# Optimization experiments

Hardware: AMD Instinct MI355X
Metric: run time of the kernel (lower is better)

Reference implementation:

```python
import jax, jax.numpy as jnp
import numpy as np

N_NODES = 16384
N_EDGES = 131072
EDGE_DIM = 16
IN_CH = 32
OUT_CH = 32
HID_EDGE = 64
MLP_HID = 64  # int(32 * 2.0)
OUT_FINAL = 10
N_GRAPHS = 64
BN_EPS = 1e-5


def setup_inputs() -> dict:
    key = jax.random.key(0)
    ks = jax.random.split(key, 20)
    s = lambda *sh: 1.0 / np.sqrt(sh[0])
    inp = {
        'x': jax.random.normal(ks[0], (N_NODES, IN_CH), jnp.float32),
        'edge_attr': jax.random.normal(ks[1], (N_EDGES, EDGE_DIM), jnp.float32),
        'edge_index': jax.random.randint(ks[2], (2, N_EDGES), 0, N_NODES, jnp.int64),
        'batch': jnp.sort(jax.random.randint(ks[3], (N_NODES,), 0, N_GRAPHS, jnp.int64)),
    }
    # layer 0: edge MLP (EDGE_DIM->HID_EDGE->IN_CH*OUT_CH), root, bias, BN affine
    inp['w1_0'] = jax.random.normal(ks[4], (EDGE_DIM, HID_EDGE), jnp.float32) * s(EDGE_DIM)
    inp['b1_0'] = jnp.zeros((HID_EDGE,), jnp.float32)
    inp['w2_0'] = jax.random.normal(ks[5], (HID_EDGE, IN_CH * OUT_CH), jnp.float32) * s(HID_EDGE)
    inp['b2_0'] = jnp.zeros((IN_CH * OUT_CH,), jnp.float32)
    inp['root_0'] = jax.random.normal(ks[6], (IN_CH, OUT_CH), jnp.float32) * s(IN_CH)
    inp['bias_0'] = jnp.zeros((OUT_CH,), jnp.float32)
    inp['gamma_0'] = jnp.ones((OUT_CH,), jnp.float32)
    inp['beta_0'] = jnp.zeros((OUT_CH,), jnp.float32)
    # layer 1: edge MLP (EDGE_DIM->HID_EDGE->OUT_CH*OUT_CH)
    inp['w1_1'] = jax.random.normal(ks[7], (EDGE_DIM, HID_EDGE), jnp.float32) * s(EDGE_DIM)
    inp['b1_1'] = jnp.zeros((HID_EDGE,), jnp.float32)
    inp['w2_1'] = jax.random.normal(ks[8], (HID_EDGE, OUT_CH * OUT_CH), jnp.float32) * s(HID_EDGE)
    inp['b2_1'] = jnp.zeros((OUT_CH * OUT_CH,), jnp.float32)
    inp['root_1'] = jax.random.normal(ks[9], (OUT_CH, OUT_CH), jnp.float32) * s(OUT_CH)
    inp['bias_1'] = jnp.zeros((OUT_CH,), jnp.float32)
    inp['gamma_1'] = jnp.ones((OUT_CH,), jnp.float32)
    inp['beta_1'] = jnp.zeros((OUT_CH,), jnp.float32)
    # final MLP (dropout is identity in eval / deterministic reference)
    inp['mlp_w1'] = jax.random.normal(ks[10], (OUT_CH, MLP_HID), jnp.float32) * s(OUT_CH)
    inp['mlp_b1'] = jnp.zeros((MLP_HID,), jnp.float32)
    inp['mlp_w2'] = jax.random.normal(ks[11], (MLP_HID, OUT_FINAL), jnp.float32) * s(MLP_HID)
    inp['mlp_b2'] = jnp.zeros((OUT_FINAL,), jnp.float32)
    return inp


def _nnconv(x, src, dst, edge_attr, w1, b1, w2, b2, root, bias, out_ch):
    # per-edge weight matrices from the edge MLP: [E, in, out]
    h = jax.nn.relu(edge_attr @ w1 + b1)
    W = (h @ w2 + b2).reshape(-1, x.shape[1], out_ch)
    msg = jnp.einsum('ei,eio->eo', x[src], W)  # gather + per-edge matmul
    agg = jax.ops.segment_sum(msg, dst, num_segments=N_NODES)
    cnt = jax.ops.segment_sum(jnp.ones((dst.shape[0], 1), x.dtype), dst, num_segments=N_NODES)
    agg = agg / jnp.maximum(cnt, 1.0)  # scatter-mean (zero-degree nodes -> 0)
    return agg + x @ root + bias


def _bn(x, gamma, beta):
    m = jnp.mean(x, axis=0)
    v = jnp.var(x, axis=0)
    return (x - m) * jax.lax.rsqrt(v + BN_EPS) * gamma + beta


def reference(x, edge_attr, edge_index, batch,
              w1_0, b1_0, w2_0, b2_0, root_0, bias_0, gamma_0, beta_0,
              w1_1, b1_1, w2_1, b2_1, root_1, bias_1, gamma_1, beta_1,
              mlp_w1, mlp_b1, mlp_w2, mlp_b2):
    src, dst = edge_index[0], edge_index[1]
    h = _nnconv(x, src, dst, edge_attr, w1_0, b1_0, w2_0, b2_0, root_0, bias_0, OUT_CH)
    h = jax.nn.relu(_bn(h, gamma_0, beta_0))
    h = _nnconv(h, src, dst, edge_attr, w1_1, b1_1, w2_1, b2_1, root_1, bias_1, OUT_CH)
    h = jax.nn.relu(_bn(h, gamma_1, beta_1))
    # global mean pool over graphs
    pooled = jax.ops.segment_sum(h, batch, num_segments=N_GRAPHS)
    gcnt = jax.ops.segment_sum(jnp.ones((h.shape[0], 1), h.dtype), batch, num_segments=N_GRAPHS)
    pooled = pooled / jnp.maximum(gcnt, 1.0)
    logits = jax.nn.relu(pooled @ mlp_w1 + mlp_b1) @ mlp_w2 + mlp_b2
    return logits
```

## Files before the change

### kernel.cpp

```cpp
#include <hip/hip_runtime.h>
#include <hip/hip_bf16.h>

#define NN 16384
#define NE 131072
#define NG 64
#define EPB 128

typedef unsigned short u16;
typedef unsigned int u32;
typedef __attribute__((ext_vector_type(8))) short short8;
typedef __attribute__((ext_vector_type(4))) float f32x4;
typedef __attribute__((ext_vector_type(8))) _Float16 f16x8;
typedef __attribute__((ext_vector_type(2))) _Float16 f16x2;
typedef __attribute__((address_space(1))) const unsigned int gu32;
typedef __attribute__((address_space(3))) unsigned int lu32;

__device__ __forceinline__ float bf2f(u16 u) {
    u32 x = ((u32)u) << 16;
    return __builtin_bit_cast(float, x);
}
__device__ __forceinline__ u16 f2bf(float f) {
    u32 u = __builtin_bit_cast(u32, f);
    u = u + 0x7fffu + ((u >> 16) & 1u);
    return (u16)(u >> 16);
}
__device__ __forceinline__ u16 f2h(float f) {
    _Float16 h = (_Float16)f;
    return __builtin_bit_cast(u16, h);
}
__device__ __forceinline__ f16x2 pkrtz(float a, float b) {
    auto v = __builtin_amdgcn_cvt_pkrtz(a, b);
    static_assert(sizeof(v) == 4, "pkrtz size");
    return __builtin_bit_cast(f16x2, v);
}
#if __has_builtin(__builtin_amdgcn_cvt_pk_bf16_f32)
__device__ __forceinline__ u32 pk2bf_fast(float a, float b) {
    auto v = __builtin_amdgcn_cvt_pk_bf16_f32(a, b);
    static_assert(sizeof(v) == 4, "cvt_pk_bf16 size");
    return __builtin_bit_cast(u32, v);
}
#else
__device__ __forceinline__ u32 pk2bf_fast(float a, float b) {
    u32 ua = __builtin_bit_cast(u32, a) + 0x8000u;
    u32 ub = __builtin_bit_cast(u32, b) + 0x8000u;
    return __builtin_amdgcn_perm(ub, ua, 0x07060302u);
}
#endif
__device__ __forceinline__ float loadF(const void* p, int i, bool bf) {
    return bf ? bf2f(((const u16*)p)[i]) : ((const float*)p)[i];
}
__device__ __forceinline__ int loadI(const void* p, int i, bool i64) {
    return i64 ? (int)((const long long*)p)[i] : ((const int*)p)[i];
}
__device__ __forceinline__ bool det_bf(const void* g0) {
    return ((const u16*)g0)[0] == 0x3F80u;
}
__device__ __forceinline__ bool det_i64(const void* eidx) {
    const u32* u = (const u32*)eidx;
    return (u[1] | u[3] | u[5] | u[7]) == 0u;
}

__global__ __launch_bounds__(256) void k_prep(const void* w2a, const void* b2a,
                                              const void* w2b, const void* b2b,
                                              const void* w1a, const void* w1b,
                                              u16* bp0, u16* bp1, u16* w1p0, u16* w1p1,
                                              const void* eidx, float* cnt, u32* eoff,
                                              const void* g0) {
    const bool bf = det_bf(g0);
    int id = blockIdx.x * 256 + threadIdx.x;
    if (id < 2 * 66560) {
        int l = id / 66560, v = id % 66560;
        int j = v & 7, lane = (v >> 3) & 63, nt = (v >> 9) & 1, t = v >> 10;
        int kk = (lane >> 4) * 8 + j;
        int n = (lane & 15) + 16 * nt;
        const void* w2 = l ? w2b : w2a;
        const void* b2 = l ? b2b : b2a;
        float val = (t < 64) ? loadF(w2, t * 1024 + kk * 32 + n, bf)
                             : loadF(b2, kk * 32 + n, bf);
        (l ? bp1 : bp0)[v] = f2h(val);
    } else if (id < 2 * 66560 + 2 * 2048) {
        int v = id - 2 * 66560;
        int l = v >> 11; v &= 2047;
        int j = v & 7, lane = (v >> 3) & 63, nt = v >> 9;
        int k = (lane >> 4) * 8 + j;
        int n = nt * 16 + (lane & 15);
        const void* w1 = l ? w1b : w1a;
        float val = (k < 16) ? loadF(w1, k * 64 + n, bf) : 0.f;
        (l ? w1p1 : w1p0)[v] = f2bf(val);
    } else {
        const bool i64 = det_i64(eidx);
        int e = id - (2 * 66560 + 2 * 2048);
        int d = loadI(eidx, NE + e, i64);
        int slot = (int)atomicAdd(&cnt[d], 1.0f);
        eoff[e] = (slot < 64) ? (u32)(d * 64 + slot) : 0xFFFFFFFFu;
    }
}

__device__ __forceinline__ void stage_chunk(const u16* Bpack, u16* lds, int cc, int w, int lane) {
    const char* src = (const char*)Bpack + (size_t)cc * 8192 + (size_t)(w * 1024 + lane * 16);
    char* dst = (char*)lds + w * 1024;
    __builtin_amdgcn_global_load_lds((gu32*)src, (lu32*)dst, 16, 0, 0);
    __builtin_amdgcn_global_load_lds((gu32*)(src + 4096), (lu32*)(dst + 4096), 16, 0, 0);
}

#define HSTR 72
__global__ __launch_bounds__(256, 4) void k_edge(const void* ea, const u16* w1p, const void* b1,
                                                 const void* xv, int layer1,
                                                 const float* sSp, const float* sQp,
                                                 const void* gammap, const void* betap,
                                                 const void* eidx, const u16* Bpack,
                                                 const u32* eoff, float* msgb, const void* g0) {
    const bool bf = det_bf(g0);
    const bool i64 = det_i64(eidx);
    __shared__ __align__(16) u16 hl[EPB * HSTR];
    __shared__ __align__(16) u16 Bls[2][4096];
    __shared__ __align__(16) float bnS[32], bnB[32];
    const int tid = threadIdx.x;
    const int e0 = blockIdx.x * EPB;
    const int lane = tid & 63;
    const int w = tid >> 6;
    const int q = lane >> 4;
    const int m = lane & 15;
    const int wbl = w * 32;
    const int wb = e0 + wbl;

    stage_chunk(Bpack, Bls[0], 0, w, lane);
    stage_chunk(Bpack, Bls[1], 1, w, lane);

    if (layer1 && tid < 32) {
        float s = 0.f, qq = 0.f;
#pragma unroll
        for (int p = 0; p < 16; p++) { s += sSp[p * 32 + tid]; qq += sQp[p * 32 + tid]; }
        float mn = s * (1.0f / 16384.0f);
        float var = qq * (1.0f / 16384.0f) - mn * mn;
        float inv = rsqrtf(var + 1e-5f);
        float g = loadF(gammap, tid, bf), b = loadF(betap, tid, bf);
        bnS[tid] = inv * g;
        bnB[tid] = b - mn * inv * g;
    }

    {
        short8 Ah[2];
#pragma unroll
        for (int e2 = 0; e2 < 2; e2++) {
            int eg = wb + e2 * 16 + m;
            uint4 av = make_uint4(0u, 0u, 0u, 0u);
            if (bf) {
                uint4 t = *(const uint4*)((const char*)ea + (size_t)eg * 32 + (q & 1) * 16);
                if (q < 2) av = t;
            } else {
                const float4* p = (const float4*)((const char*)ea + (size_t)eg * 64 + (q & 1) * 32);
                float4 a = p[0], b = p[1];
                if (q < 2) av = make_uint4(pk2bf_fast(a.x, a.y), pk2bf_fast(a.z, a.w),
                                           pk2bf_fast(b.x, b.y), pk2bf_fast(b.z, b.w));
            }
            Ah[e2] = __builtin_bit_cast(short8, av);
        }
#pragma unroll
        for (int nt = 0; nt < 4; nt++) {
            uint4 bw = *(const uint4*)&w1p[(nt * 64 + lane) * 8];
            short8 Bf = __builtin_bit_cast(short8, bw);
            float bb = loadF(b1, nt * 16 + m, bf);
#pragma unroll
            for (int e2 = 0; e2 < 2; e2++) {
                f32x4 c = __builtin_amdgcn_mfma_f32_16x16x32_bf16(
                    Ah[e2], Bf, f32x4{0.f, 0.f, 0.f, 0.f}, 0, 0, 0);
                int rbase = (wbl + e2 * 16 + q * 4) * HSTR + nt * 16 + m;
#pragma unroll
                for (int r = 0; r < 4; r++) {
                    _Float16 hv = (_Float16)fmaxf(c[r] + bb, 0.f);
                    hl[rbase + r * HSTR] = __builtin_bit_cast(u16, hv);
                }
            }
        }
    }

    float4 ga[2], gb[2];
#pragma unroll
    for (int mt = 0; mt < 2; mt++) {
        int s = loadI(eidx, wb + mt * 16 + m, i64);
        if (layer1 || !bf) {
            const float4* xp = (const float4*)xv + (size_t)s * 8 + q * 2;
            ga[mt] = xp[0]; gb[mt] = xp[1];
        } else {
            const uint4* xp = (const uint4*)((const char*)xv + (size_t)s * 64 + q * 16);
            uint4 a = *xp;
            ga[mt] = make_float4(bf2f((u16)(a.x & 0xffff)), bf2f((u16)(a.x >> 16)),
                                 bf2f((u16)(a.y & 0xffff)), bf2f((u16)(a.y >> 16)));
            gb[mt] = make_float4(bf2f((u16)(a.z & 0xffff)), bf2f((u16)(a.z >> 16)),
                                 bf2f((u16)(a.w & 0xffff)), bf2f((u16)(a.w >> 16)));
        }
    }

    __syncthreads();

    f16x2 xh[2][4];
    if (layer1) {
        float4 s0 = *(const float4*)&bnS[q * 8], s1 = *(const float4*)&bnS[q * 8 + 4];
        float4 h0 = *(const float4*)&bnB[q * 8], h1 = *(const float4*)&bnB[q * 8 + 4];
#pragma unroll
        for (int mt = 0; mt < 2; mt++) {
            xh[mt][0] = pkrtz(fmaxf(ga[mt].x * s0.x + h0.x, 0.f), fmaxf(ga[mt].y * s0.y + h0.y, 0.f));
            xh[mt][1] = pkrtz(fmaxf(ga[mt].z * s0.z + h0.z, 0.f), fmaxf(ga[mt].w * s0.w + h0.w, 0.f));
            xh[mt][2] = pkrtz(fmaxf(gb[mt].x * s1.x + h1.x, 0.f), fmaxf(gb[mt].y * s1.y + h1.y, 0.f));
            xh[mt][3] = pkrtz(fmaxf(gb[mt].z * s1.z + h1.z, 0.f), fmaxf(gb[mt].w * s1.w + h1.w, 0.f));
        }
    } else {
#pragma unroll
        for (int mt = 0; mt < 2; mt++) {
            xh[mt][0] = pkrtz(ga[mt].x, ga[mt].y);
            xh[mt][1] = pkrtz(ga[mt].z, ga[mt].w);
            xh[mt][2] = pkrtz(gb[mt].x, gb[mt].y);
            xh[mt][3] = pkrtz(gb[mt].z, gb[mt].w);
        }
    }

    f32x4 acc[2][2];
#pragma unroll
    for (int mt = 0; mt < 2; mt++) {
        acc[mt][0] = f32x4{0.f, 0.f, 0.f, 0.f};
        acc[mt][1] = f32x4{0.f, 0.f, 0.f, 0.f};
    }
    int rowb[2];
#pragma unroll
    for (int mt = 0; mt < 2; mt++) rowb[mt] = (wbl + mt * 16 + m) * HSTR;

    for (int cc = 0; cc < 16; cc++) {
        uint2 hw[2];
        hw[0] = *(const uint2*)&hl[rowb[0] + cc * 4];
        hw[1] = *(const uint2*)&hl[rowb[1] + cc * 4];
        const u16* Bb = &Bls[cc & 1][lane * 8];
#pragma unroll
        for (int tt = 0; tt < 4; tt++) {
            uint4 bu0 = *(const uint4*)(Bb + (tt * 2 + 0) * 512);
            uint4 bu1 = *(const uint4*)(Bb + (tt * 2 + 1) * 512);
            f16x8 B0 = __builtin_bit_cast(f16x8, bu0);
            f16x8 B1 = __builtin_bit_cast(f16x8, bu1);
            const u32 sel = (tt & 1) ? 0x03020302u : 0x01000100u;
#pragma unroll
            for (int mt = 0; mt < 2; mt++) {
                u32 wd = (tt & 2) ? hw[mt].y : hw[mt].x;
                u32 hh = __builtin_amdgcn_perm(wd, wd, sel);
                f16x2 h2 = __builtin_bit_cast(f16x2, hh);
                f16x2 p0 = h2 * xh[mt][0];
                f16x2 p1 = h2 * xh[mt][1];
                f16x2 p2 = h2 * xh[mt][2];
                f16x2 p3 = h2 * xh[mt][3];
                uint4 au = make_uint4(__builtin_bit_cast(u32, p0), __builtin_bit_cast(u32, p1),
                                      __builtin_bit_cast(u32, p2), __builtin_bit_cast(u32, p3));
                f16x8 A = __builtin_bit_cast(f16x8, au);
                acc[mt][0] = __builtin_amdgcn_mfma_f32_16x16x32_f16(A, B0, acc[mt][0], 0, 0, 0);
                acc[mt][1] = __builtin_amdgcn_mfma_f32_16x16x32_f16(A, B1, acc[mt][1], 0, 0, 0);
            }
        }
        __syncthreads();
        if (cc < 15) stage_chunk(Bpack, Bls[cc & 1], cc + 2, w, lane);
    }
    {
        const u16* Bb = &Bls[0][lane * 8];
        uint4 bu0 = *(const uint4*)(Bb + 0);
        uint4 bu1 = *(const uint4*)(Bb + 512);
        f16x8 B0 = __builtin_bit_cast(f16x8, bu0);
        f16x8 B1 = __builtin_bit_cast(f16x8, bu1);
#pragma unroll
        for (int mt = 0; mt < 2; mt++) {
            uint4 au = make_uint4(__builtin_bit_cast(u32, xh[mt][0]), __builtin_bit_cast(u32, xh[mt][1]),
                                  __builtin_bit_cast(u32, xh[mt][2]), __builtin_bit_cast(u32, xh[mt][3]));
            f16x8 A = __builtin_bit_cast(f16x8, au);
            acc[mt][0] = __builtin_amdgcn_mfma_f32_16x16x32_f16(A, B0, acc[mt][0], 0, 0, 0);
            acc[mt][1] = __builtin_amdgcn_mfma_f32_16x16x32_f16(A, B1, acc[mt][1], 0, 0, 0);
        }
    }

#pragma unroll
    for (int mt = 0; mt < 2; mt++) {
        int eb = wb + mt * 16 + q * 4;
#pragma unroll
        for (int r = 0; r < 4; r++) {
            u32 eo = eoff[eb + r];
            if (eo != 0xFFFFFFFFu) {
                float* mp = msgb + (size_t)eo * 32 + m;
                mp[0] = acc[mt][0][r];
                mp[16] = acc[mt][1][r];
            }
        }
    }
}

__global__ __launch_bounds__(256) void k_node(const float* msgb, const float* cnt,
                                              const void* xv, int layer1,
                                              const float* sSp, const float* sQp,
                                              const void* gammap, const void* betap,
                                              const void* root, const void* bias,
                                              float* hpre, float* sS, float* sQ,
                                              const void* g0) {
    const bool bf = det_bf(g0);
    const int tid = threadIdx.x;
    const int o = tid & 31;
    const int grp = tid >> 5;
    const int wid = tid >> 6;
    const int lane = tid & 63;
    __shared__ float bnS[32], bnB[32];
    __shared__ float partS[128], partQ[128];

    if (layer1) {
        if (tid < 32) {
            float s = 0.f, qq = 0.f;
#pragma unroll
            for (int p = 0; p < 16; p++) { s += sSp[p * 32 + tid]; qq += sQp[p * 32 + tid]; }
            float mn = s * (1.0f / 16384.0f);
            float var = qq * (1.0f / 16384.0f) - mn * mn;
            float inv = rsqrtf(var + 1e-5f);
            float g = loadF(gammap, tid, bf), b = loadF(betap, tid, bf);
            bnS[tid] = inv * g;
            bnB[tid] = b - mn * inv * g;
        }
        __syncthreads();
    }

    float Rcol[32];
#pragma unroll
    for (int i = 0; i < 32; i++) Rcol[i] = loadF(root, i * 32 + o, bf);
    const float bias_o = loadF(bias, o, bf);

    float sacc = 0.f, qacc = 0.f;
#pragma unroll
    for (int it = 0; it < 4; it++) {
        const int v = blockIdx.x * 32 + it * 8 + grp;
        float a = bias_o;
        if (layer1) {
            const float4* xp = (const float4*)((const float*)xv + (size_t)v * 32);
#pragma unroll
            for (int i = 0; i < 8; i++) {
                float4 xc = xp[i];
                a += fmaxf(xc.x * bnS[i * 4 + 0] + bnB[i * 4 + 0], 0.f) * Rcol[i * 4 + 0];
                a += fmaxf(xc.y * bnS[i * 4 + 1] + bnB[i * 4 + 1], 0.f) * Rcol[i * 4 + 1];
                a += fmaxf(xc.z * bnS[i * 4 + 2] + bnB[i * 4 + 2], 0.f) * Rcol[i * 4 + 2];
                a += fmaxf(xc.w * bnS[i * 4 + 3] + bnB[i * 4 + 3], 0.f) * Rcol[i * 4 + 3];
            }
        } else if (!bf) {
            const float4* xp = (const float4*)((const float*)xv + (size_t)v * 32);
#pragma unroll
            for (int i = 0; i < 8; i++) {
                float4 xc = xp[i];
                a += xc.x * Rcol[i * 4 + 0] + xc.y * Rcol[i * 4 + 1]
                   + xc.z * Rcol[i * 4 + 2] + xc.w * Rcol[i * 4 + 3];
            }
        } else {
            const uint4* xp = (const uint4*)((const char*)xv + (size_t)v * 64);
#pragma unroll
            for (int i = 0; i < 4; i++) {
                uint4 xc = xp[i];
                a += bf2f((u16)(xc.x & 0xffff)) * Rcol[i * 8 + 0]
                   + bf2f((u16)(xc.x >> 16))    * Rcol[i * 8 + 1]
                   + bf2f((u16)(xc.y & 0xffff)) * Rcol[i * 8 + 2]
                   + bf2f((u16)(xc.y >> 16))    * Rcol[i * 8 + 3]
                   + bf2f((u16)(xc.z & 0xffff)) * Rcol[i * 8 + 4]
                   + bf2f((u16)(xc.z >> 16))    * Rcol[i * 8 + 5]
                   + bf2f((u16)(xc.w & 0xffff)) * Rcol[i * 8 + 6]
                   + bf2f((u16)(xc.w >> 16))    * Rcol[i * 8 + 7];
            }
        }
        float cv = cnt[v];
        int deg = (int)cv;
        if (deg > 64) deg = 64;
        const float* mb = msgb + (size_t)v * 2048 + o;
        float av0 = 0.f, av1 = 0.f;
        int j = 0;
        for (; j + 1 < deg; j += 2) {
            av0 += mb[(size_t)j * 32];
            av1 += mb[(size_t)(j + 1) * 32];
        }
        if (j < deg) av0 += mb[(size_t)j * 32];
        float pre = (av0 + av1) / fmaxf(cv, 1.0f) + a;
        hpre[(size_t)v * 32 + o] = pre;
        sacc += pre;
        qacc += pre * pre;
    }

    sacc += __shfl_xor(sacc, 32, 64);
    qacc += __shfl_xor(qacc, 32, 64);
    if (lane < 32) { partS[wid * 32 + lane] = sacc; partQ[wid * 32 + lane] = qacc; }
    __syncthreads();
    if (tid < 32) {
        float ts = partS[o] + partS[32 + o] + partS[64 + o] + partS[96 + o];
        float tq = partQ[o] + partQ[32 + o] + partQ[64 + o] + partQ[96 + o];
        int slot = (blockIdx.x & 15) * 32 + o;
        atomicAdd(&sS[slot], ts);
        atomicAdd(&sQ[slot], tq);
    }
}

__global__ __launch_bounds__(256) void k_tail(const float* hpre, const float* sS, const float* sQ,
                                              const void* gamma, const void* beta,
                                              const void* batch,
                                              const void* w1, const void* b1,
                                              const void* w2, const void* b2,
                                              void* out, const void* eidx, const void* g0) {
    const bool bf = det_bf(g0);
    const bool i64 = det_i64(eidx);
    const int g = blockIdx.x;
    const int tid = threadIdx.x;
    const int o = tid & 31;
    const int c = tid >> 5;
    __shared__ float lS[256];
    __shared__ float pool[32];

    float s = 0.f, qq = 0.f;
#pragma unroll
    for (int pp = 0; pp < 16; pp++) { s += sS[pp * 32 + o]; qq += sQ[pp * 32 + o]; }
    float mn = s * (1.0f / 16384.0f);
    float var = qq * (1.0f / 16384.0f) - mn * mn;
    float inv = rsqrtf(var + 1e-5f);
    float gg = loadF(gamma, o, bf), bb = loadF(beta, o, bf);

    int lo = 0, hi = NN;
    while (lo < hi) {
        int mid = (lo + hi) >> 1;
        if (loadI(batch, mid, i64) < g) lo = mid + 1; else hi = mid;
    }
    int lo2 = lo, hi2 = NN;
    while (lo2 < hi2) {
        int mid = (lo2 + hi2) >> 1;
        if (loadI(batch, mid, i64) < g + 1) lo2 = mid + 1; else hi2 = mid;
    }
    const int nbeg = lo, nend = lo2;

    float acc = 0.f;
    for (int v = nbeg + c; v < nend; v += 8)
        acc += fmaxf((hpre[(size_t)v * 32 + o] - mn) * inv * gg + bb, 0.f);
    lS[tid] = acc;
    __syncthreads();
#pragma unroll
    for (int off = 4; off >= 1; off >>= 1) {
        if (c < off) lS[tid] += lS[tid + off * 32];
        __syncthreads();
    }
    if (tid < 32) pool[o] = lS[o] / fmaxf((float)(nend - nbeg), 1.0f);
    __syncthreads();

    if (tid < 64) {
        float a = loadF(b1, tid, bf);
#pragma unroll
        for (int i = 0; i < 32; i++) a += pool[i] * loadF(w1, i * 64 + tid, bf);
        a = fmaxf(a, 0.f);
        float lg[10];
#pragma unroll
        for (int cc = 0; cc < 10; cc++) lg[cc] = a * loadF(w2, tid * 10 + cc, bf);
#pragma unroll
        for (int off = 32; off >= 1; off >>= 1) {
#pragma unroll
            for (int cc = 0; cc < 10; cc++) lg[cc] += __shfl_down(lg[cc], off, 64);
        }
        if (tid == 0) {
            if (bf) {
                u16* op = (u16*)out;
#pragma unroll
                for (int cc = 0; cc < 10; cc++) op[g * 10 + cc] = f2bf(lg[cc] + loadF(b2, cc, bf));
            } else {
                float* op = (float*)out;
#pragma unroll
                for (int cc = 0; cc < 10; cc++) op[g * 10 + cc] = lg[cc] + loadF(b2, cc, bf);
            }
        }
    }
}

extern "C" void kernel_launch(void* const* d_in, const int* in_sizes, int n_in,
                              void* d_out, int out_size, void* d_ws, size_t ws_size,
                              hipStream_t stream) {
    char* ws = (char*)d_ws;
    u16* bp0  = (u16*)(ws + 256);
    u16* bp1  = (u16*)(ws + 256 + 133120);
    u16* w1p0 = (u16*)(ws + 266496);
    u16* w1p1 = (u16*)(ws + 270592);
    char* zbase = ws + 274688;
    float* cnt    = (float*)(zbase);
    float* sS0    = (float*)(zbase + 65536);
    float* sQ0    = (float*)(zbase + 67584);
    float* sS1    = (float*)(zbase + 69632);
    float* sQ1    = (float*)(zbase + 71680);
    const size_t zsize = 73728;
    char* nz = zbase + 73728;
    u32*   eoff  = (u32*)(nz);
    float* msgb  = (float*)(nz + 524288);
    float* hpre0 = (float*)(nz + 524288 + 134217728);
    float* hpre1 = (float*)(nz + 524288 + 134217728 + 2097152);

    const void* x     = d_in[0];
    const void* ea    = d_in[1];
    const void* eidx  = d_in[2];
    const void* batch = d_in[3];
    const void* g0    = d_in[10];

    (void)hipMemsetAsync(zbase, 0, zsize, stream);
    k_prep<<<1048, 256, 0, stream>>>(d_in[6], d_in[7], d_in[14], d_in[15],
                                     d_in[4], d_in[12],
                                     bp0, bp1, w1p0, w1p1, eidx, cnt, eoff, g0);

    k_edge<<<NE / EPB, 256, 0, stream>>>(ea, w1p0, d_in[5], x, 0,
                                         nullptr, nullptr, nullptr, nullptr,
                                         eidx, bp0, eoff, msgb, g0);
    k_node<<<NN / 32, 256, 0, stream>>>(msgb, cnt, x, 0,
                                        nullptr, nullptr, nullptr, nullptr,
                                        d_in[8], d_in[9], hpre0, sS0, sQ0, g0);

    k_edge<<<NE / EPB, 256, 0, stream>>>(ea, w1p1, d_in[13], hpre0, 1,
                                         sS0, sQ0, d_in[10], d_in[11],
                                         eidx, bp1, eoff, msgb, g0);
    k_node<<<NN / 32, 256, 0, stream>>>(msgb, cnt, hpre0, 1,
                                        sS0, sQ0, d_in[10], d_in[11],
                                        d_in[16], d_in[17], hpre1, sS1, sQ1, g0);

    k_tail<<<NG, 256, 0, stream>>>(hpre1, sS1, sQ1, d_in[18], d_in[19], batch,
                                   d_in[20], d_in[21], d_in[22], d_in[23], d_out, eidx, g0);
}
```

Baseline: 213.9 us.

## Split per-node message reduction across eight thread groups in k_node

Restructures k_node so each block handles 16 nodes. The root-weight product is computed first and staged in shared memory. The sum over incoming messages is then split across the eight 32-thread groups, which reduce through shared memory with a barrier per node. This targets the long serial loop one group ran over a high-degree node's message slots, which caused load imbalance and latency stalls. In exchange it adds 16 block barriers per block and a single-warp finalisation step.

```diff
diff --git a/kernel.cpp b/kernel.cpp
--- a/kernel.cpp
+++ b/kernel.cpp
@@ -297,18 +297,18 @@
     const bool bf = det_bf(g0);
     const int tid = threadIdx.x;
     const int o = tid & 31;
-    const int grp = tid >> 5;
+    const int s = tid >> 5;
     const int wid = tid >> 6;
-    const int lane = tid & 63;
     __shared__ float bnS[32], bnB[32];
-    __shared__ float partS[128], partQ[128];
+    __shared__ float aArr[16][32];
+    __shared__ float part[2][4][32];
 
     if (layer1) {
         if (tid < 32) {
-            float s = 0.f, qq = 0.f;
-#pragma unroll
-            for (int p = 0; p < 16; p++) { s += sSp[p * 32 + tid]; qq += sQp[p * 32 + tid]; }
-            float mn = s * (1.0f / 16384.0f);
+            float ss = 0.f, qq = 0.f;
+#pragma unroll
+            for (int p = 0; p < 16; p++) { ss += sSp[p * 32 + tid]; qq += sQp[p * 32 + tid]; }
+            float mn = ss * (1.0f / 16384.0f);
             float var = qq * (1.0f / 16384.0f) - mn * mn;
             float inv = rsqrtf(var + 1e-5f);
             float g = loadF(gammap, tid, bf), b = loadF(betap, tid, bf);
@@ -318,76 +318,81 @@
         __syncthreads();
     }
 
-    float Rcol[32];
-#pragma unroll
-    for (int i = 0; i < 32; i++) Rcol[i] = loadF(root, i * 32 + o, bf);
-    const float bias_o = loadF(bias, o, bf);
+    const int vbase = blockIdx.x * 16;
+
+    {
+        float Rcol[32];
+#pragma unroll
+        for (int i = 0; i < 32; i++) Rcol[i] = loadF(root, i * 32 + o, bf);
+        const float bias_o = loadF(bias, o, bf);
+#pragma unroll
+        for (int r = 0; r < 2; r++) {
+            const int vl = r * 8 + s;
+            const int v = vbase + vl;
+            float a = bias_o;
+            if (layer1) {
+                const float4* xp = (const float4*)((const float*)xv + (size_t)v * 32);
+#pragma unroll
+                for (int i = 0; i < 8; i++) {
+                    float4 xc = xp[i];
+                    a += fmaxf(xc.x * bnS[i * 4 + 0] + bnB[i * 4 + 0], 0.f) * Rcol[i * 4 + 0];
+                    a += fmaxf(xc.y * bnS[i * 4 + 1] + bnB[i * 4 + 1], 0.f) * Rcol[i * 4 + 1];
+                    a += fmaxf(xc.z * bnS[i * 4 + 2] + bnB[i * 4 + 2], 0.f) * Rcol[i * 4 + 2];
+                    a += fmaxf(xc.w * bnS[i * 4 + 3] + bnB[i * 4 + 3], 0.f) * Rcol[i * 4 + 3];
+                }
+            } else if (!bf) {
+                const float4* xp = (const float4*)((const float*)xv + (size_t)v * 32);
+#pragma unroll
+                for (int i = 0; i < 8; i++) {
+                    float4 xc = xp[i];
+                    a += xc.x * Rcol[i * 4 + 0] + xc.y * Rcol[i * 4 + 1]
+                       + xc.z * Rcol[i * 4 + 2] + xc.w * Rcol[i * 4 + 3];
+                }
+            } else {
+                const uint4* xp = (const uint4*)((const char*)xv + (size_t)v * 64);
+#pragma unroll
+                for (int i = 0; i < 4; i++) {
+                    uint4 xc = xp[i];
+                    a += bf2f((u16)(xc.x & 0xffff)) * Rcol[i * 8 + 0]
+                       + bf2f((u16)(xc.x >> 16))    * Rcol[i * 8 + 1]
+                       + bf2f((u16)(xc.y & 0xffff)) * Rcol[i * 8 + 2]
+                       + bf2f((u16)(xc.y >> 16))    * Rcol[i * 8 + 3]
+                       + bf2f((u16)(xc.z & 0xffff)) * Rcol[i * 8 + 4]
+                       + bf2f((u16)(xc.z >> 16))    * Rcol[i * 8 + 5]
+                       + bf2f((u16)(xc.w & 0xffff)) * Rcol[i * 8 + 6]
+                       + bf2f((u16)(xc.w >> 16))    * Rcol[i * 8 + 7];
+                }
+            }
+            aArr[vl][o] = a;
+        }
+    }
+    __syncthreads();
 
     float sacc = 0.f, qacc = 0.f;
-#pragma unroll
-    for (int it = 0; it < 4; it++) {
-        const int v = blockIdx.x * 32 + it * 8 + grp;
-        float a = bias_o;
-        if (layer1) {
-            const float4* xp = (const float4*)((const float*)xv + (size_t)v * 32);
-#pragma unroll
-            for (int i = 0; i < 8; i++) {
-                float4 xc = xp[i];
-                a += fmaxf(xc.x * bnS[i * 4 + 0] + bnB[i * 4 + 0], 0.f) * Rcol[i * 4 + 0];
-                a += fmaxf(xc.y * bnS[i * 4 + 1] + bnB[i * 4 + 1], 0.f) * Rcol[i * 4 + 1];
-                a += fmaxf(xc.z * bnS[i * 4 + 2] + bnB[i * 4 + 2], 0.f) * Rcol[i * 4 + 2];
-                a += fmaxf(xc.w * bnS[i * 4 + 3] + bnB[i * 4 + 3], 0.f) * Rcol[i * 4 + 3];
-            }
-        } else if (!bf) {
-            const float4* xp = (const float4*)((const float*)xv + (size_t)v * 32);
-#pragma unroll
-            for (int i = 0; i < 8; i++) {
-                float4 xc = xp[i];
-                a += xc.x * Rcol[i * 4 + 0] + xc.y * Rcol[i * 4 + 1]
-                   + xc.z * Rcol[i * 4 + 2] + xc.w * Rcol[i * 4 + 3];
-            }
-        } else {
-            const uint4* xp = (const uint4*)((const char*)xv + (size_t)v * 64);
-#pragma unroll
-            for (int i = 0; i < 4; i++) {
-                uint4 xc = xp[i];
-                a += bf2f((u16)(xc.x & 0xffff)) * Rcol[i * 8 + 0]
-                   + bf2f((u16)(xc.x >> 16))    * Rcol[i * 8 + 1]
-                   + bf2f((u16)(xc.y & 0xffff)) * Rcol[i * 8 + 2]
-                   + bf2f((u16)(xc.y >> 16))    * Rcol[i * 8 + 3]
-                   + bf2f((u16)(xc.z & 0xffff)) * Rcol[i * 8 + 4]
-                   + bf2f((u16)(xc.z >> 16))    * Rcol[i * 8 + 5]
-                   + bf2f((u16)(xc.w & 0xffff)) * Rcol[i * 8 + 6]
-                   + bf2f((u16)(xc.w >> 16))    * Rcol[i * 8 + 7];
-            }
-        }
-        float cv = cnt[v];
+    for (int vl = 0; vl < 16; vl++) {
+        const int v = vbase + vl;
+        const float cv = cnt[v];
         int deg = (int)cv;
         if (deg > 64) deg = 64;
-        const float* mb = msgb + (size_t)v * 2048 + o;
-        float av0 = 0.f, av1 = 0.f;
-        int j = 0;
-        for (; j + 1 < deg; j += 2) {
-            av0 += mb[(size_t)j * 32];
-            av1 += mb[(size_t)(j + 1) * 32];
-        }
-        if (j < deg) av0 += mb[(size_t)j * 32];
-        float pre = (av0 + av1) / fmaxf(cv, 1.0f) + a;
-        hpre[(size_t)v * 32 + o] = pre;
-        sacc += pre;
-        qacc += pre * pre;
-    }
-
-    sacc += __shfl_xor(sacc, 32, 64);
-    qacc += __shfl_xor(qacc, 32, 64);
-    if (lane < 32) { partS[wid * 32 + lane] = sacc; partQ[wid * 32 + lane] = qacc; }
-    __syncthreads();
+        const float* mb = msgb + (size_t)v * 2048;
+        float ps = 0.f;
+        for (int j = s; j < deg; j += 8) ps += mb[j * 32 + o];
+        ps += __shfl_xor(ps, 32, 64);
+        const int buf = vl & 1;
+        if ((tid & 63) < 32) part[buf][wid][o] = ps;
+        __syncthreads();
+        if (tid < 32) {
+            float tot = part[buf][0][o] + part[buf][1][o] + part[buf][2][o] + part[buf][3][o];
+            float pre = tot / fmaxf(cv, 1.0f) + aArr[vl][o];
+            hpre[(size_t)v * 32 + o] = pre;
+            sacc += pre;
+            qacc += pre * pre;
+        }
+    }
     if (tid < 32) {
-        float ts = partS[o] + partS[32 + o] + partS[64 + o] + partS[96 + o];
-        float tq = partQ[o] + partQ[32 + o] + partQ[64 + o] + partQ[96 + o];
-        int slot = (blockIdx.x & 15) * 32 + o;
-        atomicAdd(&sS[slot], ts);
-        atomicAdd(&sQ[slot], tq);
+        int slot = ((int)blockIdx.x & 15) * 32 + o;
+        atomicAdd(&sS[slot], sacc);
+        atomicAdd(&sQ[slot], qacc);
     }
 }
 
@@ -501,14 +506,14 @@
     k_edge<<<NE / EPB, 256, 0, stream>>>(ea, w1p0, d_in[5], x, 0,
                                          nullptr, nullptr, nullptr, nullptr,
                                          eidx, bp0, eoff, msgb, g0);
-    k_node<<<NN / 32, 256, 0, stream>>>(msgb, cnt, x, 0,
+    k_node<<<NN / 16, 256, 0, stream>>>(msgb, cnt, x, 0,
                                         nullptr, nullptr, nullptr, nullptr,
                                         d_in[8], d_in[9], hpre0, sS0, sQ0, g0);
 
     k_edge<<<NE / EPB, 256, 0, stream>>>(ea, w1p1, d_in[13], hpre0, 1,
                                          sS0, sQ0, d_in[10], d_in[11],
                                          eidx, bp1, eoff, msgb, g0);
-    k_node<<<NN / 32, 256, 0, stream>>>(msgb, cnt, hpre0, 1,
+    k_node<<<NN / 16, 256, 0, stream>>>(msgb, cnt, hpre0, 1,
                                         sS0, sQ0, d_in[10], d_in[11],
                                         d_in[16], d_in[17], hpre1, sS1, sQ1, g0);
 
```

Measured after the change: 217.6 us. No clear change (+1.7%).
